# Performance work log

Measured on AMD Instinct MI355X. Metric: run time of the kernel, lower is better.

## Reference

```python
import jax, jax.numpy as jnp
import numpy as np
from jax import lax

B, N, C_IN, C_OUT = 4, 8192, 64, 128
STRIDE, RADIUS, K, L = 4, 0.1, 32, 2
EPS = 1e-5
M = N // STRIDE


def _bn(x, g, b):
    # training-mode batch norm, channel-first layout (B, C, ...)
    axes = (0,) + tuple(range(2, x.ndim))
    mean = jnp.mean(x, axis=axes, keepdims=True)
    var = jnp.mean((x - mean) ** 2, axis=axes, keepdims=True)
    sh = (1, -1) + (1,) * (x.ndim - 2)
    return (x - mean) * lax.rsqrt(var + EPS) * g.reshape(sh) + b.reshape(sh)


def _fps(points, m):
    # farthest point sampling starting at index 0 (matches fps_cuda semantics)
    b, n, _ = points.shape
    bi = jnp.arange(b)

    def body(carry, _):
        dis, last = carry
        lp = points[bi, last]  # (b,3)
        d = jnp.sum((points - lp[:, None, :]) ** 2, -1)
        dis = jnp.minimum(dis, d)
        return (dis, jnp.argmax(dis, -1).astype(jnp.int32)), last

    init = (jnp.full((b, n), 1e10, points.dtype), jnp.zeros((b,), jnp.int32))
    _, idx = lax.scan(body, init, None, length=m)
    return idx.T  # (b, m)


def _ball_query(radius, k, centroids, points, features):
    # first k points within radius of each centroid; pad with first hit
    b, n, _ = points.shape
    d2 = jnp.sum((centroids[:, :, None, :] - points[:, None, :, :]) ** 2, -1)  # (b,m,n)
    key = jnp.where(d2 < radius * radius, jnp.arange(n, dtype=jnp.int32), n)
    neg, _ = lax.top_k(-key, k)  # k smallest keys = first k in-ball indices
    sel = -neg  # (b,m,k)
    sel = jnp.where(sel == n, sel[..., :1], sel)
    sel = jnp.clip(sel, 0, n - 1)
    bi = jnp.arange(b)[:, None, None]
    gp = jnp.transpose(points[bi, sel], (0, 3, 2, 1))  # (b,3,k,m)
    gf = None
    if features is not None:
        gf = jnp.transpose(features[bi, sel], (0, 3, 2, 1))  # (b,c,k,m)
    return gp, gf


def _forward(pos, x, p):
    b, n, _ = pos.shape
    m = n // STRIDE
    bi = jnp.arange(b)[:, None]
    fps_idx = _fps(pos, m)
    centroids = pos[bi, fps_idx]  # (b,m,3)
    # x_mlp: 1x1 conv + BN + ReLU
    f = jax.nn.relu(_bn(jnp.einsum('bnc,oc->bon', x, p['W_x']), p['g_x'], p['b_x']))
    feats = jnp.transpose(f, (0, 2, 1))  # (b,n,C_OUT)
    gp, gf = _ball_query(RADIUS, K, centroids, pos, feats)
    cT = jnp.transpose(centroids, (0, 2, 1))[:, :, None, :]  # (b,3,1,m)
    gp = (gp - cT) / RADIUS
    gp = jax.nn.relu(_bn(jnp.einsum('bckm,oc->bokm', gp, p['W_ps']), p['g_ps'], p['b_ps']))
    xf = jnp.transpose(jnp.max(gf + gp, axis=2), (0, 2, 1))  # (b,m,C_OUT)
    # gen_pe on downsampled points
    R2 = RADIUS * 2
    gpe, _ = _ball_query(R2, K, centroids, centroids, None)
    gpe = (gpe - cT) / R2
    pe = jax.nn.relu(_bn(jnp.einsum('bckm,oc->bokm', gpe, p['W_pe']), p['g_pe'], p['b_pe']))
    # InvResMLP blocks
    for i in range(L):
        xc = jnp.transpose(xf, (0, 2, 1))  # (b,C,m)
        xc = jax.nn.relu(_bn(jnp.einsum('bcm,oc->bom', xc, p['W1'][i]), p['g1'][i], p['b1'][i]))
        feats_i = jnp.transpose(xc, (0, 2, 1))  # (b,m,C)
        _, gfi = _ball_query(R2, K, centroids, centroids, feats_i)
        g = jnp.max(gfi + pe, axis=2)  # (b,C,m)
        g = jax.nn.relu(_bn(jnp.einsum('bcm,oc->bom', g, p['W2a'][i]), p['g2a'][i], p['b2a'][i]))
        g = _bn(jnp.einsum('bcm,oc->bom', g, p['W2b'][i]), p['g2b'][i], p['b2b'][i])
        xf = jax.nn.relu(feats_i + jnp.transpose(g, (0, 2, 1)))
    return centroids, xf


def setup_inputs() -> dict:
    key = jax.random.key(0)
    ks = jax.random.split(key, 12)
    d = {
        'pos': jax.random.uniform(ks[0], (B, N, 3), jnp.float32),
        'x': jax.random.normal(ks[1], (B, N, C_IN), jnp.float32),
        'W_x': jax.random.normal(ks[2], (C_OUT, C_IN), jnp.float32) * 0.05,
        'g_x': jnp.ones((C_OUT,), jnp.float32), 'b_x': jnp.zeros((C_OUT,), jnp.float32),
        'W_ps': jax.random.normal(ks[3], (C_OUT, 3), jnp.float32) * 0.1,
        'g_ps': jnp.ones((C_OUT,), jnp.float32), 'b_ps': jnp.zeros((C_OUT,), jnp.float32),
        'W_pe': jax.random.normal(ks[4], (C_OUT, 3), jnp.float32) * 0.1,
        'g_pe': jnp.ones((C_OUT,), jnp.float32), 'b_pe': jnp.zeros((C_OUT,), jnp.float32),
        'W1': jax.random.normal(ks[5], (L, C_OUT, C_OUT), jnp.float32) * 0.05,
        'g1': jnp.ones((L, C_OUT), jnp.float32), 'b1': jnp.zeros((L, C_OUT), jnp.float32),
        'W2a': jax.random.normal(ks[6], (L, C_OUT, C_OUT), jnp.float32) * 0.05,
        'g2a': jnp.ones((L, C_OUT), jnp.float32), 'b2a': jnp.zeros((L, C_OUT), jnp.float32),
        'W2b': jax.random.normal(ks[7], (L, C_OUT, C_OUT), jnp.float32) * 0.05,
        'g2b': jnp.ones((L, C_OUT), jnp.float32), 'b2b': jnp.zeros((L, C_OUT), jnp.float32),
    }
    return d


def reference(pos, x, W_x, g_x, b_x, W_ps, g_ps, b_ps, W_pe, g_pe, b_pe,
              W1, g1, b1, W2a, g2a, b2a, W2b, g2b, b2b):
    p = dict(W_x=W_x, g_x=g_x, b_x=b_x, W_ps=W_ps, g_ps=g_ps, b_ps=b_ps,
             W_pe=W_pe, g_pe=g_pe, b_pe=b_pe, W1=W1, g1=g1, b1=b1,
             W2a=W2a, g2a=g2a, b2a=b2a, W2b=W2b, g2b=g2b, b2b=b2b)
    return _forward(pos, x, p)
```

## Files before the change

### kernel.cpp

```cpp
#include <hip/hip_runtime.h>


#define BB 4
#define NN 8192
#define MM 2048
#define HM 1024
#define KK 32
#define CI 64
#define CO 128
#define SG 16

typedef float vf2 __attribute__((ext_vector_type(2)));

#define ST_X 0
#define MO_PS 256
#define MO_PE 272
#define ST1 288
#define ST2A (288 + 2 * SG * 256)
#define ST2B (ST2A + 2 * SG * 256)
#define ST_TOTAL (ST2B + 512)

__device__ __forceinline__ float sq3(float dx, float dy, float dz) {
#pragma clang fp contract(off)
  return dx * dx + dy * dy + dz * dz;
}

__device__ __forceinline__ void fin_stats_d(const double* st, float gam,
                                            float bet, double cnt, int ch,
                                            float* sc, float* sh) {
  double mean = st[ch] / cnt;
  double var = st[128 + ch] / cnt - mean * mean;
  if (var < 0) var = 0;
  double s = (double)gam / sqrt(var + 1e-5);
  *sc = (float)s;
  *sh = (float)((double)bet - mean * s);
}

__device__ __forceinline__ void fin_grp_d(const double* st, float gam,
                                          float bet, double cnt, int ch,
                                          float* sc, float* sh) {
  double sum = 0, ssq = 0;
#pragma unroll
  for (int g = 0; g < SG; g++) {
    sum += st[g * 256 + ch];
    ssq += st[g * 256 + 128 + ch];
  }
  double mean = sum / cnt;
  double var = ssq / cnt - mean * mean;
  if (var < 0) var = 0;
  double s = (double)gam / sqrt(var + 1e-5);
  *sc = (float)s;
  *sh = (float)((double)bet - mean * s);
}

__device__ __forceinline__ void fin_mom_d(const double* mo, const float* Wrow,
                                          float gam, float bet, double cnt,
                                          float* sc, float* sh) {
  double w0 = Wrow[0], w1 = Wrow[1], w2 = Wrow[2];
  double mx = mo[0] / cnt, my = mo[1] / cnt, mz = mo[2] / cnt;
  double sxx = mo[3] / cnt, sxy = mo[4] / cnt, sxz = mo[5] / cnt;
  double syy = mo[6] / cnt, syz = mo[7] / cnt, szz = mo[8] / cnt;
  double mean = w0 * mx + w1 * my + w2 * mz;
  double ey2 = w0 * w0 * sxx + w1 * w1 * syy + w2 * w2 * szz +
               2.0 * (w0 * w1 * sxy + w0 * w2 * sxz + w1 * w2 * syz);
  double var = ey2 - mean * mean;
  if (var < 0) var = 0;
  double s = (double)gam / sqrt(var + 1e-5);
  *sc = (float)s;
  *sh = (float)((double)bet - mean * s);
}

template <int CTRL>
__device__ __forceinline__ int dpp_i(int v) {
  return __builtin_amdgcn_update_dpp(v, v, CTRL, 0xF, 0xF, false);
}
template <int CTRL>
__device__ __forceinline__ float dpp_f(float v) {
  return __int_as_float(dpp_i<CTRL>(__float_as_int(v)));
}

#define FT 512
#define NP 8
#define NW 8

__device__ __forceinline__ void bq_wave(int pair, const float* __restrict__ pts,
                                        int npts, float rsq, float inv_r,
                                        int* __restrict__ sel,
                                        const float* __restrict__ cent,
                                        int lane, int* __restrict__ s_selw,
                                        float* __restrict__ s_momw) {
  int b = pair >> 11;
  const float* P = pts + (size_t)b * npts * 3;
  const float* C = cent + (size_t)pair * 3;
  float cx = C[0], cy = C[1], cz = C[2];
  int cnt = 0;
  unsigned long long ltm = (1ull << lane) - 1ull;
  int nit = npts >> 8;
  for (int ch = 0; ch < nit; ch++) {
    int i0 = (ch << 8) + lane;
    bool h0, h1, h2, h3;
    {
      float a0 = P[i0 * 3 + 0], a1 = P[i0 * 3 + 1], a2 = P[i0 * 3 + 2];
      float b0 = P[(i0 + 64) * 3 + 0], b1 = P[(i0 + 64) * 3 + 1],
            b2 = P[(i0 + 64) * 3 + 2];
      float c0 = P[(i0 + 128) * 3 + 0], c1 = P[(i0 + 128) * 3 + 1],
            c2 = P[(i0 + 128) * 3 + 2];
      float e0 = P[(i0 + 192) * 3 + 0], e1 = P[(i0 + 192) * 3 + 1],
            e2 = P[(i0 + 192) * 3 + 2];
      h0 = sq3(a0 - cx, a1 - cy, a2 - cz) < rsq;
      h1 = sq3(b0 - cx, b1 - cy, b2 - cz) < rsq;
      h2 = sq3(c0 - cx, c1 - cy, c2 - cz) < rsq;
      h3 = sq3(e0 - cx, e1 - cy, e2 - cz) < rsq;
    }
    unsigned long long m0 = __ballot(h0);
    unsigned long long m1 = __ballot(h1);
    unsigned long long m2 = __ballot(h2);
    unsigned long long m3 = __ballot(h3);
    if (m0) {
      int k = cnt + __popcll(m0 & ltm);
      if (h0 && k < KK) s_selw[k] = i0;
      cnt += __popcll(m0);
    }
    if (m1) {
      int k = cnt + __popcll(m1 & ltm);
      if (h1 && k < KK) s_selw[k] = i0 + 64;
      cnt += __popcll(m1);
    }
    if (m2) {
      int k = cnt + __popcll(m2 & ltm);
      if (h2 && k < KK) s_selw[k] = i0 + 128;
      cnt += __popcll(m2);
    }
    if (m3) {
      int k = cnt + __popcll(m3 & ltm);
      if (h3 && k < KK) s_selw[k] = i0 + 192;
      cnt += __popcll(m3);
    }
    if (cnt >= KK) break;
  }
  int total = cnt < KK ? cnt : KK;
  int myidx = 0;
  if (lane < KK) {
    int v = (lane < total) ? s_selw[lane] : s_selw[0];
    sel[(size_t)pair * KK + lane] = v;
    myidx = v;
  }
  float gx = 0.f, gy = 0.f, gz = 0.f;
  if (lane < KK) {
    gx = (P[myidx * 3 + 0] - cx) * inv_r;
    gy = (P[myidx * 3 + 1] - cy) * inv_r;
    gz = (P[myidx * 3 + 2] - cz) * inv_r;
  }
  float v9[9] = {gx, gy, gz, gx * gx, gx * gy, gx * gz, gy * gy, gy * gz,
                 gz * gz};
#pragma unroll
  for (int j = 0; j < 9; j++) {
#pragma unroll
    for (int off = 32; off > 0; off >>= 1) v9[j] += __shfl_xor(v9[j], off);
  }
  if (lane == 0) {
#pragma unroll
    for (int j = 0; j < 9; j++) s_momw[j] = v9[j];
  }
}

__global__ __launch_bounds__(FT) void k_fps_conv(
    const float* __restrict__ pos, const float* __restrict__ x,
    const float* __restrict__ W_x, float* __restrict__ cent,
    float* __restrict__ fpre, double* __restrict__ stats,
    float* __restrict__ gds) {
  __shared__ alignas(16) unsigned long long s_key[2][NW];
  __shared__ alignas(16) float s_pts[NN * 3];
  __shared__ alignas(16) float s_cent[MM * 3];
  int t = threadIdx.x;
  if (blockIdx.x >= BB) {
    int cb = blockIdx.x - BB;
    int o = t & 127, q = t >> 7;
    float4 w[CI / 4];
    const float4* Wv = (const float4*)(W_x + (size_t)o * CI);
#pragma unroll
    for (int i = 0; i < CI / 4; i++) w[i] = Wv[i];
    int row0 = cb * 128;
    float ssum = 0.f, ssq = 0.f;
    for (int r = 0; r < 128; r += 4) {
      int row = __builtin_amdgcn_readfirstlane(row0 + r + q);
      const float* xr = x + (size_t)row * CI;
      float acc = 0.f;
#pragma unroll
      for (int i = 0; i < CI / 4; i++) {
        float4 a = *(const float4*)(xr + 4 * i);
        acc += a.x * w[i].x + a.y * w[i].y + a.z * w[i].z + a.w * w[i].w;
      }
      fpre[(size_t)row * CO + o] = acc;
      ssum += acc;
      ssq += acc * acc;
    }
    atomicAdd(&stats[ST_X + o], (double)ssum);
    atomicAdd(&stats[ST_X + 128 + o], (double)ssq);
    return;
  }
  int b = blockIdx.x;
  const float* P = pos + (size_t)b * NN * 3;
  float* C = cent + (size_t)b * MM * 3;
  int lane = t & 63, w = t >> 6;
  int ws = __builtin_amdgcn_readfirstlane(w);
  for (int i = t; i < (NN * 3) / 4; i += FT) {
    ((float4*)s_pts)[i] = ((const float4*)P)[i];
  }
  vf2 px[NP], py[NP], pz[NP], ds[NP];
#pragma unroll
  for (int s = 0; s < NP; s++) {
    int ia = (2 * s) * FT + t;
    int ib = ia + FT;
    px[s] = (vf2){P[ia * 3 + 0], P[ib * 3 + 0]};
    py[s] = (vf2){P[ia * 3 + 1], P[ib * 3 + 1]};
    pz[s] = (vf2){P[ia * 3 + 2], P[ib * 3 + 2]};
    ds[s] = (vf2){1e10f, 1e10f};
  }
  float lx = P[0], ly = P[1], lz = P[2];
  if (t == 0) {
    s_cent[0] = lx;
    s_cent[1] = ly;
    s_cent[2] = lz;
  }
  __syncthreads();
  for (int m = 1; m < HM; m++) {
    vf2 l2x = (vf2){lx, lx}, l2y = (vf2){ly, ly}, l2z = (vf2){lz, lz};
    vf2 bmax = (vf2){-1.0f, -1.0f};
    {
#pragma clang fp contract(off)
#pragma unroll
      for (int s = 0; s < NP; s++) {
        vf2 dx = px[s] - l2x;
        vf2 dy = py[s] - l2y;
        vf2 dz = pz[s] - l2z;
        vf2 d2 = dx * dx + dy * dy + dz * dz;
        vf2 nd = __builtin_elementwise_min(ds[s], d2);
        ds[s] = nd;
        bmax = __builtin_elementwise_max(bmax, nd);
      }
    }
    float bv = fmaxf(bmax.x, bmax.y);
    bv = fmaxf(bv, dpp_f<0x111>(bv));
    bv = fmaxf(bv, dpp_f<0x112>(bv));
    bv = fmaxf(bv, dpp_f<0x114>(bv));
    bv = fmaxf(bv, dpp_f<0x118>(bv));
    bv = fmaxf(bv, dpp_f<0x142>(bv));
    bv = fmaxf(bv, dpp_f<0x143>(bv));
    float wmax =
        __int_as_float(__builtin_amdgcn_readlane(__float_as_int(bv), 63));
    unsigned idxw = 0xffffffffu;
#pragma unroll
    for (int s = NP - 1; s >= 0; s--) {
      unsigned long long mby = __ballot(ds[s].y == wmax);
      unsigned basey = (unsigned)((2 * s) * FT + FT + (ws << 6));
      if (mby) idxw = basey + (unsigned)(__ffsll((long long)mby) - 1);
      unsigned long long mbx = __ballot(ds[s].x == wmax);
      unsigned basex = (unsigned)((2 * s) * FT + (ws << 6));
      if (mbx) idxw = basex + (unsigned)(__ffsll((long long)mbx) - 1);
    }
    int pb = m & 1;
    if (lane == 0) {
      s_key[pb][ws] = ((unsigned long long)__float_as_uint(wmax) << 32) |
                      (unsigned long long)(~idxw);
    }
    __syncthreads();
    const ulonglong2* kp = (const ulonglong2*)(&s_key[pb][0]);
    ulonglong2 q0 = kp[0];
    ulonglong2 q1 = kp[1];
    ulonglong2 q2 = kp[2];
    ulonglong2 q3 = kp[3];
    unsigned long long a0 = q0.x > q0.y ? q0.x : q0.y;
    unsigned long long a1 = q1.x > q1.y ? q1.x : q1.y;
    unsigned long long a2 = q2.x > q2.y ? q2.x : q2.y;
    unsigned long long a3 = q3.x > q3.y ? q3.x : q3.y;
    a0 = a0 > a1 ? a0 : a1;
    a2 = a2 > a3 ? a2 : a3;
    unsigned long long kw = a0 > a2 ? a0 : a2;
    unsigned gidx = ~(unsigned)(kw & 0xffffffffull);
    lx = s_pts[gidx * 3 + 0];
    ly = s_pts[gidx * 3 + 1];
    lz = s_pts[gidx * 3 + 2];
    if (t == 0) {
      s_cent[m * 3 + 0] = lx;
      s_cent[m * 3 + 1] = ly;
      s_cent[m * 3 + 2] = lz;
    }
  }
  __syncthreads();
  for (int i = t; i < (HM * 3) / 4; i += FT) {
    ((float4*)C)[i] = ((const float4*)s_cent)[i];
  }
  float2* gd = (float2*)gds + (size_t)b * NP * FT;
#pragma unroll
  for (int s = 0; s < NP; s++) {
    float2 v;
    v.x = ds[s].x;
    v.y = ds[s].y;
    gd[s * FT + t] = v;
  }
}

__global__ __launch_bounds__(FT) void k_fps_bq(const float* __restrict__ pos,
                                               float* __restrict__ cent,
                                               const float* __restrict__ gds,
                                               int* __restrict__ sel1,
                                               double* __restrict__ stats) {
  __shared__ alignas(16) unsigned long long s_key[2][NW];
  __shared__ alignas(16) float s_pts[NN * 3];
  __shared__ alignas(16) float s_cent[MM * 3];
  __shared__ int s_sel[NW][KK];
  __shared__ float s_mom[NW][9];
  int t = threadIdx.x;
  int lane = t & 63, w = t >> 6;
  if (blockIdx.x >= BB) {
    int pi = (blockIdx.x - BB) * 8 + w;
    int bb = pi >> 10, mi = pi & (HM - 1);
    int pair = bb * MM + mi;
    bq_wave(pair, pos, NN, 0.01f, 10.0f, sel1, cent, lane, s_sel[w],
            s_mom[w]);
    __syncthreads();
    if (t < 9) {
      double a = (double)s_mom[0][t];
#pragma unroll
      for (int j = 1; j < NW; j++) a += s_mom[j][t];
      atomicAdd(&stats[MO_PS + t], a);
    }
    return;
  }
  int b = blockIdx.x;
  const float* P = pos + (size_t)b * NN * 3;
  float* C = cent + (size_t)b * MM * 3;
  int ws = __builtin_amdgcn_readfirstlane(w);
  for (int i = t; i < (NN * 3) / 4; i += FT) {
    ((float4*)s_pts)[i] = ((const float4*)P)[i];
  }
  vf2 px[NP], py[NP], pz[NP], ds[NP];
  const float2* gd = (const float2*)gds + (size_t)b * NP * FT;
#pragma unroll
  for (int s = 0; s < NP; s++) {
    int ia = (2 * s) * FT + t;
    int ib = ia + FT;
    px[s] = (vf2){P[ia * 3 + 0], P[ib * 3 + 0]};
    py[s] = (vf2){P[ia * 3 + 1], P[ib * 3 + 1]};
    pz[s] = (vf2){P[ia * 3 + 2], P[ib * 3 + 2]};
    float2 v = gd[s * FT + t];
    ds[s] = (vf2){v.x, v.y};
  }
  float lx = C[(HM - 1) * 3 + 0];
  float ly = C[(HM - 1) * 3 + 1];
  float lz = C[(HM - 1) * 3 + 2];
  __syncthreads();
  for (int m = HM; m < MM; m++) {
    vf2 l2x = (vf2){lx, lx}, l2y = (vf2){ly, ly}, l2z = (vf2){lz, lz};
    vf2 bmax = (vf2){-1.0f, -1.0f};
    {
#pragma clang fp contract(off)
#pragma unroll
      for (int s = 0; s < NP; s++) {
        vf2 dx = px[s] - l2x;
        vf2 dy = py[s] - l2y;
        vf2 dz = pz[s] - l2z;
        vf2 d2 = dx * dx + dy * dy + dz * dz;
        vf2 nd = __builtin_elementwise_min(ds[s], d2);
        ds[s] = nd;
        bmax = __builtin_elementwise_max(bmax, nd);
      }
    }
    float bv = fmaxf(bmax.x, bmax.y);
    bv = fmaxf(bv, dpp_f<0x111>(bv));
    bv = fmaxf(bv, dpp_f<0x112>(bv));
    bv = fmaxf(bv, dpp_f<0x114>(bv));
    bv = fmaxf(bv, dpp_f<0x118>(bv));
    bv = fmaxf(bv, dpp_f<0x142>(bv));
    bv = fmaxf(bv, dpp_f<0x143>(bv));
    float wmax =
        __int_as_float(__builtin_amdgcn_readlane(__float_as_int(bv), 63));
    unsigned idxw = 0xffffffffu;
#pragma unroll
    for (int s = NP - 1; s >= 0; s--) {
      unsigned long long mby = __ballot(ds[s].y == wmax);
      unsigned basey = (unsigned)((2 * s) * FT + FT + (ws << 6));
      if (mby) idxw = basey + (unsigned)(__ffsll((long long)mby) - 1);
      unsigned long long mbx = __ballot(ds[s].x == wmax);
      unsigned basex = (unsigned)((2 * s) * FT + (ws << 6));
      if (mbx) idxw = basex + (unsigned)(__ffsll((long long)mbx) - 1);
    }
    int pb = m & 1;
    if (lane == 0) {
      s_key[pb][ws] = ((unsigned long long)__float_as_uint(wmax) << 32) |
                      (unsigned long long)(~idxw);
    }
    __syncthreads();
    const ulonglong2* kp = (const ulonglong2*)(&s_key[pb][0]);
    ulonglong2 q0 = kp[0];
    ulonglong2 q1 = kp[1];
    ulonglong2 q2 = kp[2];
    ulonglong2 q3 = kp[3];
    unsigned long long a0 = q0.x > q0.y ? q0.x : q0.y;
    unsigned long long a1 = q1.x > q1.y ? q1.x : q1.y;
    unsigned long long a2 = q2.x > q2.y ? q2.x : q2.y;
    unsigned long long a3 = q3.x > q3.y ? q3.x : q3.y;
    a0 = a0 > a1 ? a0 : a1;
    a2 = a2 > a3 ? a2 : a3;
    unsigned long long kw = a0 > a2 ? a0 : a2;
    unsigned gidx = ~(unsigned)(kw & 0xffffffffull);
    lx = s_pts[gidx * 3 + 0];
    ly = s_pts[gidx * 3 + 1];
    lz = s_pts[gidx * 3 + 2];
    if (t == 0) {
      s_cent[m * 3 + 0] = lx;
      s_cent[m * 3 + 1] = ly;
      s_cent[m * 3 + 2] = lz;
    }
  }
  __syncthreads();
  for (int i = t + (HM * 3) / 4; i < (MM * 3) / 4; i += FT) {
    ((float4*)C)[i] = ((const float4*)s_cent)[i];
  }
}

__global__ __launch_bounds__(256) void k_bq_rest(const float* __restrict__ pos,
                                                 const float* __restrict__ cent,
                                                 int* __restrict__ sel1,
                                                 int* __restrict__ sel2,
                                                 double* __restrict__ stats) {
  __shared__ int s_sel[4][KK];
  __shared__ float s_mom[4][9];
  int t = threadIdx.x, lane = t & 63, w = t >> 6;
  const float* pts;
  int npts, pair, mo;
  float rsq, inv_r;
  int* sel;
  if (blockIdx.x < (BB * HM) / 4) {
    int pi = blockIdx.x * 4 + w;
    int bb = pi >> 10, mi = pi & (HM - 1);
    pair = bb * MM + HM + mi;
    pts = pos;
    npts = NN;
    rsq = 0.01f;
    inv_r = 10.0f;
    sel = sel1;
    mo = MO_PS;
  } else {
    pair = (blockIdx.x - (BB * HM) / 4) * 4 + w;
    pts = cent;
    npts = MM;
    rsq = 0.04f;
    inv_r = 5.0f;
    sel = sel2;
    mo = MO_PE;
  }
  bq_wave(pair, pts, npts, rsq, inv_r, sel, cent, lane, s_sel[w], s_mom[w]);
  __syncthreads();
  if (t < 9) {
    double a = (double)s_mom[0][t] + s_mom[1][t] + s_mom[2][t] + s_mom[3][t];
    atomicAdd(&stats[mo + t], a);
  }
}

__global__ __launch_bounds__(128) void k_xf_conv1(
    const float* __restrict__ pos, const float* __restrict__ cent,
    const int* __restrict__ sel1, const float* __restrict__ fpre,
    const float* __restrict__ Wps, const float* __restrict__ g_ps,
    const float* __restrict__ b_ps, const float* __restrict__ g_x,
    const float* __restrict__ b_x, const double* __restrict__ stats,
    const float* __restrict__ W1, float* __restrict__ y1a,
    double* __restrict__ st1out) {
  int pair = blockIdx.x;
  int b = pair >> 11;
  int o = threadIdx.x;
  float sx, hx, sp, hp;
  fin_stats_d(stats + ST_X, g_x[o], b_x[o], (double)(BB * NN), o, &sx, &hx);
  fin_mom_d(stats + MO_PS, Wps + o * 3, g_ps[o], b_ps[o],
            (double)(BB * MM * KK), &sp, &hp);
  float w0 = Wps[o * 3 + 0], w1 = Wps[o * 3 + 1], w2 = Wps[o * 3 + 2];
  const float* C = cent + (size_t)pair * 3;
  float cx = C[0], cy = C[1], cz = C[2];
  const float* P = pos + (size_t)b * NN * 3;
  const float* F = fpre + (size_t)b * NN * CO;
  __shared__ int s_idx[KK];
  __shared__ float s_xf[128];
  if (o < KK) s_idx[o] = sel1[(size_t)pair * KK + o];
  __syncthreads();
  float acc = -1e30f;
#pragma unroll 4
  for (int k = 0; k < KK; k++) {
    int idx = __builtin_amdgcn_readfirstlane(s_idx[k]);
    float gx = (P[idx * 3 + 0] - cx) * 10.0f;
    float gy = (P[idx * 3 + 1] - cy) * 10.0f;
    float gz = (P[idx * 3 + 2] - cz) * 10.0f;
    float y = fmaxf((w0 * gx + w1 * gy + w2 * gz) * sp + hp, 0.f);
    float f = fmaxf(F[(size_t)idx * CO + o] * sx + hx, 0.f);
    float v = y + f;
    acc = v > acc ? v : acc;
  }
  s_xf[o] = acc;
  __syncthreads();
  const float4* Wv = (const float4*)(W1 + (size_t)o * CO);
  const float4* gv = (const float4*)s_xf;
  float dot = 0.f;
#pragma unroll
  for (int i = 0; i < CO / 4; i++) {
    float4 a = gv[i];
    float4 ww = Wv[i];
    dot += a.x * ww.x + a.y * ww.y + a.z * ww.z + a.w * ww.w;
  }
  y1a[(size_t)pair * CO + o] = dot;
  int grp = pair & (SG - 1);
  atomicAdd(&st1out[grp * 256 + o], (double)dot);
  atomicAdd(&st1out[grp * 256 + 128 + o], (double)(dot * dot));
}

__global__ __launch_bounds__(256) void k_conv_bnin(
    const float* __restrict__ in, const float* __restrict__ W,
    const double* __restrict__ st_grp, const float* __restrict__ gam,
    const float* __restrict__ bet, float* __restrict__ out,
    double* __restrict__ stats, int rows_per_block) {
  __shared__ float s_sc[128], s_sh[128];
  int t = threadIdx.x;
  if (t < 128) {
    fin_grp_d(st_grp, gam[t], bet[t], (double)(BB * MM), t, &s_sc[t],
              &s_sh[t]);
  }
  __syncthreads();
  int o = t & 127, half = t >> 7;
  float4 w[CO / 4];
  const float4* Wv = (const float4*)(W + (size_t)o * CO);
#pragma unroll
  for (int i = 0; i < CO / 4; i++) w[i] = Wv[i];
  int row0 = blockIdx.x * rows_per_block;
  float ssum = 0.f, ssq = 0.f;
  for (int r = 0; r < rows_per_block; r += 2) {
    int row = __builtin_amdgcn_readfirstlane(row0 + r + half);
    const float* xr = in + (size_t)row * CO;
    float acc = 0.f;
#pragma unroll
    for (int i = 0; i < CO / 4; i++) {
      float4 a = *(const float4*)(xr + 4 * i);
      a.x = fmaxf(a.x * s_sc[4 * i + 0] + s_sh[4 * i + 0], 0.f);
      a.y = fmaxf(a.y * s_sc[4 * i + 1] + s_sh[4 * i + 1], 0.f);
      a.z = fmaxf(a.z * s_sc[4 * i + 2] + s_sh[4 * i + 2], 0.f);
      a.w = fmaxf(a.w * s_sc[4 * i + 3] + s_sh[4 * i + 3], 0.f);
      acc += a.x * w[i].x + a.y * w[i].y + a.z * w[i].z + a.w * w[i].w;
    }
    out[(size_t)row * CO + o] = acc;
    ssum += acc;
    ssq += acc * acc;
  }
  atomicAdd(&stats[o], (double)ssum);
  atomicAdd(&stats[128 + o], (double)ssq);
}

__global__ __launch_bounds__(256) void k_conv_resid(
    const float* __restrict__ y1prev, const float* __restrict__ y2bprev,
    const double* __restrict__ st1p, const float* __restrict__ g1p,
    const float* __restrict__ b1p, const double* __restrict__ st2bp,
    const float* __restrict__ g2bp, const float* __restrict__ b2bp,
    const float* __restrict__ W, float* __restrict__ y1out,
    double* __restrict__ stats, int rows_per_block) {
  __shared__ float s_s1[128], s_h1[128], s_s2[128], s_h2[128];
  int t = threadIdx.x;
  if (t < 128) {
    fin_grp_d(st1p, g1p[t], b1p[t], (double)(BB * MM), t, &s_s1[t], &s_h1[t]);
    fin_stats_d(st2bp, g2bp[t], b2bp[t], (double)(BB * MM), t, &s_s2[t],
                &s_h2[t]);
  }
  __syncthreads();
  int o = t & 127, half = t >> 7;
  float4 w[CO / 4];
  const float4* Wv = (const float4*)(W + (size_t)o * CO);
#pragma unroll
  for (int i = 0; i < CO / 4; i++) w[i] = Wv[i];
  int row0 = blockIdx.x * rows_per_block;
  float ssum = 0.f, ssq = 0.f;
  for (int r = 0; r < rows_per_block; r += 2) {
    int row = __builtin_amdgcn_readfirstlane(row0 + r + half);
    const float* ar = y1prev + (size_t)row * CO;
    const float* br = y2bprev + (size_t)row * CO;
    float acc = 0.f;
#pragma unroll
    for (int i = 0; i < CO / 4; i++) {
      float4 a = *(const float4*)(ar + 4 * i);
      float4 bb = *(const float4*)(br + 4 * i);
      float x0 = fmaxf(fmaxf(a.x * s_s1[4 * i + 0] + s_h1[4 * i + 0], 0.f) +
                           (bb.x * s_s2[4 * i + 0] + s_h2[4 * i + 0]), 0.f);
      float x1 = fmaxf(fmaxf(a.y * s_s1[4 * i + 1] + s_h1[4 * i + 1], 0.f) +
                           (bb.y * s_s2[4 * i + 1] + s_h2[4 * i + 1]), 0.f);
      float x2 = fmaxf(fmaxf(a.z * s_s1[4 * i + 2] + s_h1[4 * i + 2], 0.f) +
                           (bb.z * s_s2[4 * i + 2] + s_h2[4 * i + 2]), 0.f);
      float x3 = fmaxf(fmaxf(a.w * s_s1[4 * i + 3] + s_h1[4 * i + 3], 0.f) +
                           (bb.w * s_s2[4 * i + 3] + s_h2[4 * i + 3]), 0.f);
      acc += x0 * w[i].x + x1 * w[i].y + x2 * w[i].z + x3 * w[i].w;
    }
    y1out[(size_t)row * CO + o] = acc;
    ssum += acc;
    ssq += acc * acc;
  }
  int grp = blockIdx.x & (SG - 1);
  atomicAdd(&stats[grp * 256 + o], (double)ssum);
  atomicAdd(&stats[grp * 256 + 128 + o], (double)ssq);
}

__global__ __launch_bounds__(128) void k_gconv(
    const float* __restrict__ cent, const int* __restrict__ sel2,
    const float* __restrict__ y1in, const double* __restrict__ st1,
    const float* __restrict__ g1v, const float* __restrict__ b1v,
    const double* __restrict__ mo_pe, const float* __restrict__ Wpe,
    const float* __restrict__ gpe, const float* __restrict__ bpe,
    const float* __restrict__ W2a, float* __restrict__ y2a,
    double* __restrict__ st2a) {
  int pair = blockIdx.x;
  int b = pair >> 11;
  int o = threadIdx.x;
  float s1, h1, se, he;
  fin_grp_d(st1, g1v[o], b1v[o], (double)(BB * MM), o, &s1, &h1);
  fin_mom_d(mo_pe, Wpe + o * 3, gpe[o], bpe[o], (double)(BB * MM * KK), &se,
            &he);
  float w0 = Wpe[o * 3 + 0], w1 = Wpe[o * 3 + 1], w2 = Wpe[o * 3 + 2];
  const float* C = cent + (size_t)pair * 3;
  float cx = C[0], cy = C[1], cz = C[2];
  const float* CB = cent + (size_t)b * MM * 3;
  const float* Y = y1in + (size_t)b * MM * CO;
  __shared__ int s_idx[KK];
  __shared__ float s_g[128];
  if (o < KK) s_idx[o] = sel2[(size_t)pair * KK + o];
  __syncthreads();
  float acc = -1e30f;
#pragma unroll 4
  for (int k = 0; k < KK; k++) {
    int idx = __builtin_amdgcn_readfirstlane(s_idx[k]);
    float gx = (CB[idx * 3 + 0] - cx) * 5.0f;
    float gy = (CB[idx * 3 + 1] - cy) * 5.0f;
    float gz = (CB[idx * 3 + 2] - cz) * 5.0f;
    float pe = fmaxf((w0 * gx + w1 * gy + w2 * gz) * se + he, 0.f);
    float f = fmaxf(Y[(size_t)idx * CO + o] * s1 + h1, 0.f);
    float v = pe + f;
    acc = v > acc ? v : acc;
  }
  s_g[o] = acc;
  __syncthreads();
  const float4* Wv = (const float4*)(W2a + (size_t)o * CO);
  const float4* gv = (const float4*)s_g;
  float dot = 0.f;
#pragma unroll
  for (int i = 0; i < CO / 4; i++) {
    float4 a = gv[i];
    float4 ww = Wv[i];
    dot += a.x * ww.x + a.y * ww.y + a.z * ww.z + a.w * ww.w;
  }
  y2a[(size_t)pair * CO + o] = dot;
  int grp = pair & (SG - 1);
  atomicAdd(&st2a[grp * 256 + o], (double)dot);
  atomicAdd(&st2a[grp * 256 + 128 + o], (double)(dot * dot));
}

__global__ __launch_bounds__(256) void k_resid_fin(
    const float* __restrict__ y1b, const double* __restrict__ st1,
    const float* __restrict__ g1v, const float* __restrict__ b1v,
    const float* __restrict__ y2b, const double* __restrict__ st2b,
    const float* __restrict__ g2bv, const float* __restrict__ b2bv,
    float* __restrict__ xf) {
  int i = blockIdx.x * 256 + threadIdx.x;
  int o = i & 127;
  float s1, h1, s2, h2;
  fin_grp_d(st1, g1v[o], b1v[o], (double)(BB * MM), o, &s1, &h1);
  fin_stats_d(st2b, g2bv[o], b2bv[o], (double)(BB * MM), o, &s2, &h2);
  float f = fmaxf(y1b[i] * s1 + h1, 0.f);
  float v = y2b[i] * s2 + h2;
  xf[i] = fmaxf(f + v, 0.f);
}

extern "C" void kernel_launch(void* const* d_in, const int* in_sizes, int n_in,
                              void* d_out, int out_size, void* d_ws,
                              size_t ws_size, hipStream_t stream) {
  const float* pos = (const float*)d_in[0];
  const float* x = (const float*)d_in[1];
  const float* W_x = (const float*)d_in[2];
  const float* g_x = (const float*)d_in[3];
  const float* b_x = (const float*)d_in[4];
  const float* W_ps = (const float*)d_in[5];
  const float* g_ps = (const float*)d_in[6];
  const float* b_ps = (const float*)d_in[7];
  const float* W_pe = (const float*)d_in[8];
  const float* g_pe = (const float*)d_in[9];
  const float* b_pe = (const float*)d_in[10];
  const float* W1 = (const float*)d_in[11];
  const float* g1 = (const float*)d_in[12];
  const float* b1 = (const float*)d_in[13];
  const float* W2a = (const float*)d_in[14];
  const float* g2a = (const float*)d_in[15];
  const float* b2a = (const float*)d_in[16];
  const float* W2b = (const float*)d_in[17];
  const float* g2b = (const float*)d_in[18];
  const float* b2b = (const float*)d_in[19];

  float* cent = (float*)d_out;
  float* xf = cent + (size_t)BB * MM * 3;

  char* p = (char*)d_ws;
  double* stats = (double*)p; p += (size_t)ST_TOTAL * sizeof(double);
  int* sel1 = (int*)p;        p += (size_t)BB * MM * KK * sizeof(int);
  int* sel2 = (int*)p;        p += (size_t)BB * MM * KK * sizeof(int);
  float* fpre = (float*)p;    p += (size_t)BB * NN * CO * sizeof(float);
  float* y1a = (float*)p;     p += (size_t)BB * MM * CO * sizeof(float);
  float* y1b = (float*)p;     p += (size_t)BB * MM * CO * sizeof(float);
  float* y2a = (float*)p;     p += (size_t)BB * MM * CO * sizeof(float);
  float* y2b = (float*)p;     p += (size_t)BB * MM * CO * sizeof(float);
  float* gds = (float*)p;     p += (size_t)BB * NP * FT * 2 * sizeof(float);

  hipMemsetAsync(stats, 0, (size_t)ST_TOTAL * sizeof(double), stream);
  k_fps_conv<<<BB + 256, FT, 0, stream>>>(pos, x, W_x, cent, fpre, stats, gds);
  k_fps_bq<<<BB + (BB * HM) / 8, FT, 0, stream>>>(pos, cent, gds, sel1, stats);
  k_bq_rest<<<(BB * HM) / 4 + (BB * MM) / 4, 256, 0, stream>>>(pos, cent, sel1,
                                                               sel2, stats);
  k_xf_conv1<<<BB * MM, 128, 0, stream>>>(pos, cent, sel1, fpre, W_ps, g_ps,
                                          b_ps, g_x, b_x, stats, W1, y1a,
                                          stats + ST1);
  k_gconv<<<BB * MM, 128, 0, stream>>>(cent, sel2, y1a, stats + ST1, g1, b1,
                                       stats + MO_PE, W_pe, g_pe, b_pe, W2a,
                                       y2a, stats + ST2A);
  k_conv_bnin<<<128, 256, 0, stream>>>(y2a, W2b, stats + ST2A, g2a, b2a, y2b,
                                       stats + ST2B, 64);
  k_conv_resid<<<128, 256, 0, stream>>>(
      y1a, y2b, stats + ST1, g1, b1, stats + ST2B, g2b, b2b, W1 + CO * CO, y1b,
      stats + ST1 + SG * 256, 64);
  k_gconv<<<BB * MM, 128, 0, stream>>>(cent, sel2, y1b, stats + ST1 + SG * 256,
                                       g1 + 128, b1 + 128, stats + MO_PE, W_pe,
                                       g_pe, b_pe, W2a + CO * CO, y2a,
                                       stats + ST2A + SG * 256);
  k_conv_bnin<<<128, 256, 0, stream>>>(y2a, W2b + CO * CO,
                                       stats + ST2A + SG * 256, g2a + 128,
                                       b2a + 128, y2b, stats + ST2B + 256, 64);
  k_resid_fin<<<(BB * MM * CO) / 256, 256, 0, stream>>>(
      y1b, stats + ST1 + SG * 256, g1 + 128, b1 + 128, y2b,
      stats + ST2B + 256, g2b + 128, b2b + 128, xf);
}
```

Measured before the change: 2.544 ms.

## Split FPS into three stages to overlap more ball-query work with sampling

Farthest point sampling now runs in three segments (0-768, 768-1408, 1408-2048) instead of two halves. The middle kernel saves the running distance state to the workspace so the last kernel can resume from it. Each FPS kernel runs ball queries for the centroids already produced, so only the final 640 centroids per batch are left for the tail kernel. This hides more ball-query work behind the serial FPS loop, at the cost of one extra launch and an extra save and reload of the distance state.

```diff
diff --git a/kernel.cpp b/kernel.cpp
--- a/kernel.cpp
+++ b/kernel.cpp
@@ -4,7 +4,8 @@
 #define BB 4
 #define NN 8192
 #define MM 2048
-#define HM 1024
+#define S1 768
+#define S2 1408
 #define KK 32
 #define CI 64
 #define CO 128
@@ -224,7 +225,7 @@
     s_cent[2] = lz;
   }
   __syncthreads();
-  for (int m = 1; m < HM; m++) {
+  for (int m = 1; m < S1; m++) {
     vf2 l2x = (vf2){lx, lx}, l2y = (vf2){ly, ly}, l2z = (vf2){lz, lz};
     vf2 bmax = (vf2){-1.0f, -1.0f};
     {
@@ -288,7 +289,7 @@
     }
   }
   __syncthreads();
-  for (int i = t; i < (HM * 3) / 4; i += FT) {
+  for (int i = t; i < (S1 * 3) / 4; i += FT) {
     ((float4*)C)[i] = ((const float4*)s_cent)[i];
   }
   float2* gd = (float2*)gds + (size_t)b * NP * FT;
@@ -301,11 +302,11 @@
   }
 }
 
-__global__ __launch_bounds__(FT) void k_fps_bq(const float* __restrict__ pos,
-                                               float* __restrict__ cent,
-                                               const float* __restrict__ gds,
-                                               int* __restrict__ sel1,
-                                               double* __restrict__ stats) {
+__global__ __launch_bounds__(FT) void k_fps_bq(
+    const float* __restrict__ pos, float* __restrict__ cent,
+    float* __restrict__ gds, int* __restrict__ sel1,
+    double* __restrict__ stats, int mStart, int mEnd, int bqBase,
+    int bqCount) {
   __shared__ alignas(16) unsigned long long s_key[2][NW];
   __shared__ alignas(16) float s_pts[NN * 3];
   __shared__ alignas(16) float s_cent[MM * 3];
@@ -315,7 +316,8 @@
   int lane = t & 63, w = t >> 6;
   if (blockIdx.x >= BB) {
     int pi = (blockIdx.x - BB) * 8 + w;
-    int bb = pi >> 10, mi = pi & (HM - 1);
+    int bb = pi / bqCount;
+    int mi = pi - bb * bqCount + bqBase;
     int pair = bb * MM + mi;
     bq_wave(pair, pos, NN, 0.01f, 10.0f, sel1, cent, lane, s_sel[w],
             s_mom[w]);
@@ -336,7 +338,7 @@
     ((float4*)s_pts)[i] = ((const float4*)P)[i];
   }
   vf2 px[NP], py[NP], pz[NP], ds[NP];
-  const float2* gd = (const float2*)gds + (size_t)b * NP * FT;
+  float2* gd = (float2*)gds + (size_t)b * NP * FT;
 #pragma unroll
   for (int s = 0; s < NP; s++) {
     int ia = (2 * s) * FT + t;
@@ -347,11 +349,11 @@
     float2 v = gd[s * FT + t];
     ds[s] = (vf2){v.x, v.y};
   }
-  float lx = C[(HM - 1) * 3 + 0];
-  float ly = C[(HM - 1) * 3 + 1];
-  float lz = C[(HM - 1) * 3 + 2];
-  __syncthreads();
-  for (int m = HM; m < MM; m++) {
+  float lx = C[(mStart - 1) * 3 + 0];
+  float ly = C[(mStart - 1) * 3 + 1];
+  float lz = C[(mStart - 1) * 3 + 2];
+  __syncthreads();
+  for (int m = mStart; m < mEnd; m++) {
     vf2 l2x = (vf2){lx, lx}, l2y = (vf2){ly, ly}, l2z = (vf2){lz, lz};
     vf2 bmax = (vf2){-1.0f, -1.0f};
     {
@@ -415,8 +417,17 @@
     }
   }
   __syncthreads();
-  for (int i = t + (HM * 3) / 4; i < (MM * 3) / 4; i += FT) {
+  for (int i = t + (mStart * 3) / 4; i < (mEnd * 3) / 4; i += FT) {
     ((float4*)C)[i] = ((const float4*)s_cent)[i];
+  }
+  if (mEnd < MM) {
+#pragma unroll
+    for (int s = 0; s < NP; s++) {
+      float2 v;
+      v.x = ds[s].x;
+      v.y = ds[s].y;
+      gd[s * FT + t] = v;
+    }
   }
 }
 
@@ -432,10 +443,12 @@
   int npts, pair, mo;
   float rsq, inv_r;
   int* sel;
-  if (blockIdx.x < (BB * HM) / 4) {
+  const int LC = MM - S2;
+  if (blockIdx.x < (BB * LC) / 4) {
     int pi = blockIdx.x * 4 + w;
-    int bb = pi >> 10, mi = pi & (HM - 1);
-    pair = bb * MM + HM + mi;
+    int bb = pi / LC;
+    int mi = pi - bb * LC + S2;
+    pair = bb * MM + mi;
     pts = pos;
     npts = NN;
     rsq = 0.01f;
@@ -443,7 +456,7 @@
     sel = sel1;
     mo = MO_PS;
   } else {
-    pair = (blockIdx.x - (BB * HM) / 4) * 4 + w;
+    pair = (blockIdx.x - (BB * LC) / 4) * 4 + w;
     pts = cent;
     npts = MM;
     rsq = 0.04f;
@@ -711,9 +724,12 @@
 
   hipMemsetAsync(stats, 0, (size_t)ST_TOTAL * sizeof(double), stream);
   k_fps_conv<<<BB + 256, FT, 0, stream>>>(pos, x, W_x, cent, fpre, stats, gds);
-  k_fps_bq<<<BB + (BB * HM) / 8, FT, 0, stream>>>(pos, cent, gds, sel1, stats);
-  k_bq_rest<<<(BB * HM) / 4 + (BB * MM) / 4, 256, 0, stream>>>(pos, cent, sel1,
-                                                               sel2, stats);
+  k_fps_bq<<<BB + (BB * S1) / 8, FT, 0, stream>>>(pos, cent, gds, sel1, stats,
+                                                  S1, S2, 0, S1);
+  k_fps_bq<<<BB + (BB * (S2 - S1)) / 8, FT, 0, stream>>>(
+      pos, cent, gds, sel1, stats, S2, MM, S1, S2 - S1);
+  k_bq_rest<<<(BB * (MM - S2)) / 4 + (BB * MM) / 4, 256, 0, stream>>>(
+      pos, cent, sel1, sel2, stats);
   k_xf_conv1<<<BB * MM, 128, 0, stream>>>(pos, cent, sel1, fpre, W_ps, g_ps,
                                           b_ps, g_x, b_x, stats, W1, y1a,
                                           stats + ST1);
```

Measured after the change: 2.554 ms. Within noise of the previous version (+0.4%).

## Replace brute-force ball query with uniform-grid binned neighbor search

Applied to the files above, without the earlier changes.

Points and centroids are bucketed into uniform 3D grids whose cell size equals the query radius, using counting sort with shared-memory atomics. Each ball query then scans only the neighboring cells instead of the whole cloud. Hits go into a per-wave buffer and are rank-sorted by original index, which preserves the first-k semantics. If a wave collects more than the buffer capacity, it falls back to a linear scan. The binning hardcodes a [0,1)^3 coordinate range and adds an extra launch plus extra workspace.

```diff
diff --git a/kernel.cpp b/kernel.cpp
--- a/kernel.cpp
+++ b/kernel.cpp
@@ -9,6 +9,7 @@
 #define CI 64
 #define CO 128
 #define SG 16
+#define CAPH 192
 
 typedef float vf2 __attribute__((ext_vector_type(2)));
 
@@ -83,62 +84,73 @@
 #define NP 8
 #define NW 8
 
-__device__ __forceinline__ void bq_wave(int pair, const float* __restrict__ pts,
-                                        int npts, float rsq, float inv_r,
-                                        int* __restrict__ sel,
-                                        const float* __restrict__ cent,
-                                        int lane, int* __restrict__ s_selw,
-                                        float* __restrict__ s_momw) {
-  int b = pair >> 11;
-  const float* P = pts + (size_t)b * npts * 3;
+__device__ __forceinline__ void bq_grid(
+    int pair, const float* __restrict__ pts, int npts,
+    const float4* __restrict__ gxyz, const int* __restrict__ gstart, int G,
+    float gs, float rad, float rsq, float inv_r, int* __restrict__ sel,
+    const float* __restrict__ cent, int lane, int* __restrict__ s_hitw,
+    int* __restrict__ s_selw, float* __restrict__ s_momw) {
   const float* C = cent + (size_t)pair * 3;
   float cx = C[0], cy = C[1], cz = C[2];
+  unsigned long long ltm = (1ull << lane) - 1ull;
+  int x0 = (int)((cx - rad - 1e-5f) * gs); x0 = x0 < 0 ? 0 : x0;
+  int x1 = (int)((cx + rad + 1e-5f) * gs); x1 = x1 > G - 1 ? G - 1 : x1;
+  int y0 = (int)((cy - rad - 1e-5f) * gs); y0 = y0 < 0 ? 0 : y0;
+  int y1 = (int)((cy + rad + 1e-5f) * gs); y1 = y1 > G - 1 ? G - 1 : y1;
+  int z0 = (int)((cz - rad - 1e-5f) * gs); z0 = z0 < 0 ? 0 : z0;
+  int z1 = (int)((cz + rad + 1e-5f) * gs); z1 = z1 > G - 1 ? G - 1 : z1;
   int cnt = 0;
-  unsigned long long ltm = (1ull << lane) - 1ull;
-  int nit = npts >> 8;
-  for (int ch = 0; ch < nit; ch++) {
-    int i0 = (ch << 8) + lane;
-    bool h0, h1, h2, h3;
-    {
-      float a0 = P[i0 * 3 + 0], a1 = P[i0 * 3 + 1], a2 = P[i0 * 3 + 2];
-      float b0 = P[(i0 + 64) * 3 + 0], b1 = P[(i0 + 64) * 3 + 1],
-            b2 = P[(i0 + 64) * 3 + 2];
-      float c0 = P[(i0 + 128) * 3 + 0], c1 = P[(i0 + 128) * 3 + 1],
-            c2 = P[(i0 + 128) * 3 + 2];
-      float e0 = P[(i0 + 192) * 3 + 0], e1 = P[(i0 + 192) * 3 + 1],
-            e2 = P[(i0 + 192) * 3 + 2];
-      h0 = sq3(a0 - cx, a1 - cy, a2 - cz) < rsq;
-      h1 = sq3(b0 - cx, b1 - cy, b2 - cz) < rsq;
-      h2 = sq3(c0 - cx, c1 - cy, c2 - cz) < rsq;
-      h3 = sq3(e0 - cx, e1 - cy, e2 - cz) < rsq;
-    }
-    unsigned long long m0 = __ballot(h0);
-    unsigned long long m1 = __ballot(h1);
-    unsigned long long m2 = __ballot(h2);
-    unsigned long long m3 = __ballot(h3);
-    if (m0) {
-      int k = cnt + __popcll(m0 & ltm);
-      if (h0 && k < KK) s_selw[k] = i0;
-      cnt += __popcll(m0);
-    }
-    if (m1) {
-      int k = cnt + __popcll(m1 & ltm);
-      if (h1 && k < KK) s_selw[k] = i0 + 64;
-      cnt += __popcll(m1);
-    }
-    if (m2) {
-      int k = cnt + __popcll(m2 & ltm);
-      if (h2 && k < KK) s_selw[k] = i0 + 128;
-      cnt += __popcll(m2);
-    }
-    if (m3) {
-      int k = cnt + __popcll(m3 & ltm);
-      if (h3 && k < KK) s_selw[k] = i0 + 192;
-      cnt += __popcll(m3);
-    }
-    if (cnt >= KK) break;
-  }
-  int total = cnt < KK ? cnt : KK;
+  for (int zz = z0; zz <= z1; zz++) {
+    for (int yy = y0; yy <= y1; yy++) {
+      int brow = (zz * G + yy) * G;
+      int sbeg = gstart[brow + x0];
+      int send = gstart[brow + x1 + 1];
+      for (int base = sbeg; base < send; base += 64) {
+        int j = base + lane;
+        bool h = false;
+        int pi = 0;
+        if (j < send) {
+          float4 v = gxyz[j];
+          pi = __float_as_int(v.w);
+          h = sq3(v.x - cx, v.y - cy, v.z - cz) < rsq;
+        }
+        unsigned long long mb = __ballot(h);
+        if (mb) {
+          int k = cnt + __popcll(mb & ltm);
+          if (h && k < CAPH) s_hitw[k] = pi;
+          cnt += __popcll(mb);
+        }
+      }
+    }
+  }
+  __syncthreads();
+  int total;
+  if (cnt <= CAPH) {
+    for (int l = lane; l < cnt; l += 64) {
+      int v = s_hitw[l];
+      int rk = 0;
+      for (int j = 0; j < cnt; j++) rk += (s_hitw[j] < v);
+      if (rk < KK) s_selw[rk] = v;
+    }
+    total = cnt < KK ? cnt : KK;
+  } else {
+    int bcnt = 0;
+    int nit = npts >> 6;
+    for (int ch = 0; ch < nit; ch++) {
+      int i0 = (ch << 6) + lane;
+      float a0 = pts[i0 * 3 + 0], a1 = pts[i0 * 3 + 1], a2 = pts[i0 * 3 + 2];
+      bool h = sq3(a0 - cx, a1 - cy, a2 - cz) < rsq;
+      unsigned long long mb = __ballot(h);
+      if (mb) {
+        int k = bcnt + __popcll(mb & ltm);
+        if (h && k < KK) s_selw[k] = i0;
+        bcnt += __popcll(mb);
+      }
+      if (bcnt >= KK) break;
+    }
+    total = bcnt < KK ? bcnt : KK;
+  }
+  __syncthreads();
   int myidx = 0;
   if (lane < KK) {
     int v = (lane < total) ? s_selw[lane] : s_selw[0];
@@ -147,9 +159,9 @@
   }
   float gx = 0.f, gy = 0.f, gz = 0.f;
   if (lane < KK) {
-    gx = (P[myidx * 3 + 0] - cx) * inv_r;
-    gy = (P[myidx * 3 + 1] - cy) * inv_r;
-    gz = (P[myidx * 3 + 2] - cz) * inv_r;
+    gx = (pts[myidx * 3 + 0] - cx) * inv_r;
+    gy = (pts[myidx * 3 + 1] - cy) * inv_r;
+    gz = (pts[myidx * 3 + 2] - cz) * inv_r;
   }
   float v9[9] = {gx, gy, gz, gx * gx, gx * gy, gx * gz, gy * gy, gy * gz,
                  gz * gz};
@@ -168,19 +180,57 @@
     const float* __restrict__ pos, const float* __restrict__ x,
     const float* __restrict__ W_x, float* __restrict__ cent,
     float* __restrict__ fpre, double* __restrict__ stats,
-    float* __restrict__ gds) {
+    float* __restrict__ gds, int* __restrict__ pg_start,
+    float4* __restrict__ pg_xyz) {
   __shared__ alignas(16) unsigned long long s_key[2][NW];
   __shared__ alignas(16) float s_pts[NN * 3];
   __shared__ alignas(16) float s_cent[MM * 3];
   int t = threadIdx.x;
+  if (blockIdx.x >= BB + 256) {
+    int bb = blockIdx.x - (BB + 256);
+    const float* P = pos + (size_t)bb * NN * 3;
+    int* cb = (int*)s_pts;
+    int* rb = cb + 1024;
+    for (int i = t; i < 1000; i += FT) cb[i] = 0;
+    __syncthreads();
+    for (int i = t; i < NN; i += FT) {
+      float px = P[i * 3 + 0], py = P[i * 3 + 1], pz = P[i * 3 + 2];
+      int bx = (int)(px * 10.f); bx = bx > 9 ? 9 : bx;
+      int by = (int)(py * 10.f); by = by > 9 ? 9 : by;
+      int bz = (int)(pz * 10.f); bz = bz > 9 ? 9 : bz;
+      atomicAdd(&cb[(bz * 10 + by) * 10 + bx], 1);
+    }
+    __syncthreads();
+    if (t == 0) {
+      int acc = 0;
+      for (int j = 0; j < 1000; j++) {
+        pg_start[bb * 1024 + j] = acc;
+        rb[j] = acc;
+        acc += cb[j];
+      }
+      pg_start[bb * 1024 + 1000] = acc;
+    }
+    __syncthreads();
+    for (int i = t; i < NN; i += FT) {
+      float px = P[i * 3 + 0], py = P[i * 3 + 1], pz = P[i * 3 + 2];
+      int bx = (int)(px * 10.f); bx = bx > 9 ? 9 : bx;
+      int by = (int)(py * 10.f); by = by > 9 ? 9 : by;
+      int bz = (int)(pz * 10.f); bz = bz > 9 ? 9 : bz;
+      int slot = atomicAdd(&rb[(bz * 10 + by) * 10 + bx], 1);
+      float4 v;
+      v.x = px; v.y = py; v.z = pz; v.w = __int_as_float(i);
+      pg_xyz[(size_t)bb * NN + slot] = v;
+    }
+    return;
+  }
   if (blockIdx.x >= BB) {
-    int cb = blockIdx.x - BB;
+    int cb2 = blockIdx.x - BB;
     int o = t & 127, q = t >> 7;
     float4 w[CI / 4];
     const float4* Wv = (const float4*)(W_x + (size_t)o * CI);
 #pragma unroll
     for (int i = 0; i < CI / 4; i++) w[i] = Wv[i];
-    int row0 = cb * 128;
+    int row0 = cb2 * 128;
     float ssum = 0.f, ssq = 0.f;
     for (int r = 0; r < 128; r += 4) {
       int row = __builtin_amdgcn_readfirstlane(row0 + r + q);
@@ -301,14 +351,15 @@
   }
 }
 
-__global__ __launch_bounds__(FT) void k_fps_bq(const float* __restrict__ pos,
-                                               float* __restrict__ cent,
-                                               const float* __restrict__ gds,
-                                               int* __restrict__ sel1,
-                                               double* __restrict__ stats) {
+__global__ __launch_bounds__(FT) void k_fps_bq(
+    const float* __restrict__ pos, float* __restrict__ cent,
+    const float* __restrict__ gds, int* __restrict__ sel1,
+    double* __restrict__ stats, const int* __restrict__ pg_start,
+    const float4* __restrict__ pg_xyz) {
   __shared__ alignas(16) unsigned long long s_key[2][NW];
   __shared__ alignas(16) float s_pts[NN * 3];
   __shared__ alignas(16) float s_cent[MM * 3];
+  __shared__ int s_hit[NW][CAPH];
   __shared__ int s_sel[NW][KK];
   __shared__ float s_mom[NW][9];
   int t = threadIdx.x;
@@ -317,8 +368,9 @@
     int pi = (blockIdx.x - BB) * 8 + w;
     int bb = pi >> 10, mi = pi & (HM - 1);
     int pair = bb * MM + mi;
-    bq_wave(pair, pos, NN, 0.01f, 10.0f, sel1, cent, lane, s_sel[w],
-            s_mom[w]);
+    bq_grid(pair, pos + (size_t)bb * NN * 3, NN, pg_xyz + (size_t)bb * NN,
+            pg_start + bb * 1024, 10, 10.f, 0.1f, 0.01f, 10.f, sel1, cent,
+            lane, s_hit[w], s_sel[w], s_mom[w]);
     __syncthreads();
     if (t < 9) {
       double a = (double)s_mom[0][t];
@@ -420,38 +472,72 @@
   }
 }
 
-__global__ __launch_bounds__(256) void k_bq_rest(const float* __restrict__ pos,
-                                                 const float* __restrict__ cent,
-                                                 int* __restrict__ sel1,
-                                                 int* __restrict__ sel2,
-                                                 double* __restrict__ stats) {
+__global__ __launch_bounds__(256) void k_bin_cent(const float* __restrict__ cent,
+                                                  int* __restrict__ cg_start,
+                                                  float4* __restrict__ cg_xyz) {
+  __shared__ int cb[128], rb[128];
+  int t = threadIdx.x, bb = blockIdx.x;
+  const float* C = cent + (size_t)bb * MM * 3;
+  for (int i = t; i < 125; i += 256) cb[i] = 0;
+  __syncthreads();
+  for (int i = t; i < MM; i += 256) {
+    float px = C[i * 3 + 0], py = C[i * 3 + 1], pz = C[i * 3 + 2];
+    int bx = (int)(px * 5.f); bx = bx > 4 ? 4 : bx;
+    int by = (int)(py * 5.f); by = by > 4 ? 4 : by;
+    int bz = (int)(pz * 5.f); bz = bz > 4 ? 4 : bz;
+    atomicAdd(&cb[(bz * 5 + by) * 5 + bx], 1);
+  }
+  __syncthreads();
+  if (t == 0) {
+    int acc = 0;
+    for (int j = 0; j < 125; j++) {
+      cg_start[bb * 128 + j] = acc;
+      rb[j] = acc;
+      acc += cb[j];
+    }
+    cg_start[bb * 128 + 125] = acc;
+  }
+  __syncthreads();
+  for (int i = t; i < MM; i += 256) {
+    float px = C[i * 3 + 0], py = C[i * 3 + 1], pz = C[i * 3 + 2];
+    int bx = (int)(px * 5.f); bx = bx > 4 ? 4 : bx;
+    int by = (int)(py * 5.f); by = by > 4 ? 4 : by;
+    int bz = (int)(pz * 5.f); bz = bz > 4 ? 4 : bz;
+    int slot = atomicAdd(&rb[(bz * 5 + by) * 5 + bx], 1);
+    float4 v;
+    v.x = px; v.y = py; v.z = pz; v.w = __int_as_float(i);
+    cg_xyz[(size_t)bb * MM + slot] = v;
+  }
+}
+
+__global__ __launch_bounds__(256) void k_bq_rest(
+    const float* __restrict__ pos, const float* __restrict__ cent,
+    const int* __restrict__ pg_start, const float4* __restrict__ pg_xyz,
+    const int* __restrict__ cg_start, const float4* __restrict__ cg_xyz,
+    int* __restrict__ sel1, int* __restrict__ sel2,
+    double* __restrict__ stats) {
+  __shared__ int s_hit[4][CAPH];
   __shared__ int s_sel[4][KK];
   __shared__ float s_mom[4][9];
   int t = threadIdx.x, lane = t & 63, w = t >> 6;
-  const float* pts;
-  int npts, pair, mo;
-  float rsq, inv_r;
-  int* sel;
-  if (blockIdx.x < (BB * HM) / 4) {
+  int mo;
+  if (blockIdx.x < (BB * (MM - HM)) / 4) {
     int pi = blockIdx.x * 4 + w;
-    int bb = pi >> 10, mi = pi & (HM - 1);
-    pair = bb * MM + HM + mi;
-    pts = pos;
-    npts = NN;
-    rsq = 0.01f;
-    inv_r = 10.0f;
-    sel = sel1;
+    int bb = pi >> 10;
+    int mi = (pi & (HM - 1)) + HM;
+    int pair = bb * MM + mi;
+    bq_grid(pair, pos + (size_t)bb * NN * 3, NN, pg_xyz + (size_t)bb * NN,
+            pg_start + bb * 1024, 10, 10.f, 0.1f, 0.01f, 10.f, sel1, cent,
+            lane, s_hit[w], s_sel[w], s_mom[w]);
     mo = MO_PS;
   } else {
-    pair = (blockIdx.x - (BB * HM) / 4) * 4 + w;
-    pts = cent;
-    npts = MM;
-    rsq = 0.04f;
-    inv_r = 5.0f;
-    sel = sel2;
+    int pi = (blockIdx.x - (BB * (MM - HM)) / 4) * 4 + w;
+    int bb = pi >> 11;
+    bq_grid(pi, cent + (size_t)bb * MM * 3, MM, cg_xyz + (size_t)bb * MM,
+            cg_start + bb * 128, 5, 5.f, 0.2f, 0.04f, 5.f, sel2, cent, lane,
+            s_hit[w], s_sel[w], s_mom[w]);
     mo = MO_PE;
   }
-  bq_wave(pair, pts, npts, rsq, inv_r, sel, cent, lane, s_sel[w], s_mom[w]);
   __syncthreads();
   if (t < 9) {
     double a = (double)s_mom[0][t] + s_mom[1][t] + s_mom[2][t] + s_mom[3][t];
@@ -708,12 +794,19 @@
   float* y2a = (float*)p;     p += (size_t)BB * MM * CO * sizeof(float);
   float* y2b = (float*)p;     p += (size_t)BB * MM * CO * sizeof(float);
   float* gds = (float*)p;     p += (size_t)BB * NP * FT * 2 * sizeof(float);
+  float4* pg_xyz = (float4*)p; p += (size_t)BB * NN * sizeof(float4);
+  float4* cg_xyz = (float4*)p; p += (size_t)BB * MM * sizeof(float4);
+  int* pg_start = (int*)p;    p += (size_t)BB * 1024 * sizeof(int);
+  int* cg_start = (int*)p;    p += (size_t)BB * 128 * sizeof(int);
 
   hipMemsetAsync(stats, 0, (size_t)ST_TOTAL * sizeof(double), stream);
-  k_fps_conv<<<BB + 256, FT, 0, stream>>>(pos, x, W_x, cent, fpre, stats, gds);
-  k_fps_bq<<<BB + (BB * HM) / 8, FT, 0, stream>>>(pos, cent, gds, sel1, stats);
-  k_bq_rest<<<(BB * HM) / 4 + (BB * MM) / 4, 256, 0, stream>>>(pos, cent, sel1,
-                                                               sel2, stats);
+  k_fps_conv<<<BB + 256 + BB, FT, 0, stream>>>(pos, x, W_x, cent, fpre, stats,
+                                               gds, pg_start, pg_xyz);
+  k_fps_bq<<<BB + (BB * HM) / 8, FT, 0, stream>>>(pos, cent, gds, sel1, stats,
+                                                  pg_start, pg_xyz);
+  k_bin_cent<<<BB, 256, 0, stream>>>(cent, cg_start, cg_xyz);
+  k_bq_rest<<<(BB * (MM - HM)) / 4 + (BB * MM) / 4, 256, 0, stream>>>(
+      pos, cent, pg_start, pg_xyz, cg_start, cg_xyz, sel1, sel2, stats);
   k_xf_conv1<<<BB * MM, 128, 0, stream>>>(pos, cent, sel1, fpre, W_ps, g_ps,
                                           b_ps, g_x, b_x, stats, W1, y1a,
                                           stats + ST1);
```

Result: no change. 2.547 ms (+0.1%).
